# Performance work log

Hardware: AMD Instinct MI355X
Metric: run time of the kernel (lower is better)

## Reference

```python
import jax, jax.numpy as jnp
import numpy as np

D_MODEL = 512
NUM_HEADS = 8
HEAD_DIM = D_MODEL // NUM_HEADS
MAX_REL = 2


def setup_inputs() -> dict:
    key = jax.random.key(0)
    ks = jax.random.split(key, 12)
    B, S = 2, 4096
    std = 1.0 / np.sqrt(D_MODEL)
    inp = {
        'q': jax.random.normal(ks[0], (B, S, D_MODEL), jnp.float32),
        'k': jax.random.normal(ks[1], (B, S, D_MODEL), jnp.float32),
        'v': jax.random.normal(ks[2], (B, S, D_MODEL), jnp.float32),
        'Wq': jax.random.normal(ks[3], (D_MODEL, D_MODEL), jnp.float32) * std,
        'bq': jnp.zeros((D_MODEL,), jnp.float32),
        'Wk': jax.random.normal(ks[4], (D_MODEL, D_MODEL), jnp.float32) * std,
        'bk': jnp.zeros((D_MODEL,), jnp.float32),
        'Wv': jax.random.normal(ks[5], (D_MODEL, D_MODEL), jnp.float32) * std,
        'bv': jnp.zeros((D_MODEL,), jnp.float32),
        'Wo': jax.random.normal(ks[6], (D_MODEL, D_MODEL), jnp.float32) * std,
        'bo': jnp.zeros((D_MODEL,), jnp.float32),
        'rel_pos': jax.random.normal(ks[7], (NUM_HEADS, 2 * MAX_REL + 1), jnp.float32),
    }
    return inp


def _rel_bias(rel_pos, seq_len):
    pos = jnp.arange(seq_len)
    rel = pos[None, :] - pos[:, None]              # [S,S]
    idx = jnp.clip(rel, -MAX_REL, MAX_REL) + MAX_REL
    return rel_pos[:, idx]                         # [H,S,S]


def reference(q, k, v, Wq, bq, Wk, bk, Wv, bv, Wo, bo, rel_pos):
    B, S, D = q.shape
    H, Hd = NUM_HEADS, HEAD_DIM
    # torch Linear: x @ W.T + b
    Q = (q @ Wq.T + bq).reshape(B, S, H, Hd).transpose(0, 2, 1, 3)  # [B,H,S,Hd]
    K = (k @ Wk.T + bk).reshape(B, S, H, Hd).transpose(0, 2, 1, 3)
    V = (v @ Wv.T + bv).reshape(B, S, H, Hd).transpose(0, 2, 1, 3)
    scores = jnp.einsum('bhqd,bhkd->bhqk', Q, K) / jnp.sqrt(jnp.float32(Hd))
    scores = scores + _rel_bias(rel_pos, S)[None]                  # [B,H,S,S]
    probs = jax.nn.softmax(scores, axis=-1)
    attn = jnp.einsum('bhqk,bhkd->bhqd', probs, V)                 # [B,H,S,Hd]
    attn = attn.transpose(0, 2, 1, 3).reshape(B, S, D)
    return attn @ Wo.T + bo
```

## Files before the change

kernel.cpp:

```cpp
#include <hip/hip_runtime.h>

typedef __bf16 bf16_t;
typedef __bf16 bf16x2 __attribute__((ext_vector_type(2)));
typedef __bf16 bf16x4 __attribute__((ext_vector_type(4)));
typedef __bf16 bf16x8 __attribute__((ext_vector_type(8)));
typedef float f32x4 __attribute__((ext_vector_type(4)));
typedef unsigned int u32x4 __attribute__((ext_vector_type(4)));

#define MFMA16(a, b, c) __builtin_amdgcn_mfma_f32_16x16x32_bf16(a, b, c, 0, 0, 0)
#define LOG2E 1.4426950408889634f
#define SHIFT 16.0f

#define GLL(g, l)                                                      \
  __builtin_amdgcn_global_load_lds(                                    \
      (const __attribute__((address_space(1))) void*)(g),              \
      (__attribute__((address_space(3))) void*)(l), 16, 0, 0)

#define WAIT_BARRIER_V4() asm volatile("s_waitcnt vmcnt(4)\n\ts_barrier" ::: "memory")
#define WAIT_BARRIER_V6() asm volatile("s_waitcnt vmcnt(6)\n\ts_barrier" ::: "memory")

static constexpr int NB = 2;
static constexpr int SEQ = 4096;
static constexpr int DM = 512;
static constexpr int NH = 8;
static constexpr int HD = 64;
static constexpr int M_ROWS = NB * SEQ;

__global__ __launch_bounds__(256) void cvt_w_kernel(
    const float* __restrict__ w0, const float* __restrict__ w1,
    const float* __restrict__ w2, const float* __restrict__ w3,
    bf16_t* __restrict__ out) {
  const float* src = (blockIdx.y == 0) ? w0 : (blockIdx.y == 1) ? w1
                   : (blockIdx.y == 2) ? w2 : w3;
  int i = (blockIdx.x * 256 + threadIdx.x) * 4;
  float4 v = *(const float4*)(src + i);
  bf16_t* o = out + blockIdx.y * (DM * DM) + i;
  o[0] = (bf16_t)v.x; o[1] = (bf16_t)v.y; o[2] = (bf16_t)v.z; o[3] = (bf16_t)v.w;
}

__global__ __launch_bounds__(256) void cvt_x_kernel(
    const float* __restrict__ q, const float* __restrict__ k,
    const float* __restrict__ v, bf16_t* __restrict__ out) {
  const float* src = (blockIdx.y == 0) ? q : (blockIdx.y == 1) ? k : v;
  bf16_t* dst = out + (size_t)blockIdx.y * (M_ROWS * DM);
  int i = (blockIdx.x * 256 + threadIdx.x) * 8;
  float4 a = *(const float4*)(src + i);
  float4 b = *(const float4*)(src + i + 4);
  bf16x8 o;
  o[0] = (bf16_t)a.x; o[1] = (bf16_t)a.y; o[2] = (bf16_t)a.z; o[3] = (bf16_t)a.w;
  o[4] = (bf16_t)b.x; o[5] = (bf16_t)b.y; o[6] = (bf16_t)b.z; o[7] = (bf16_t)b.w;
  *(bf16x8*)(dst + i) = o;
}

__device__ __forceinline__ void gemm_body64(
    const bf16_t* __restrict__ X, const bf16_t* __restrict__ Wm,
    const float* __restrict__ bias, void* __restrict__ Out,
    int omode, float scale) {
  __shared__ bf16_t Asm[3][64 * 64];
  __shared__ bf16_t Bsm[3][128 * 64];

  const int tid = threadIdx.x;
  const int w = tid >> 6;
  const int lane = tid & 63;
  const int quad = lane >> 4, l15 = lane & 15;
  const int l8 = lane >> 3;
  const int swcol = ((lane & 7) ^ l8) * 8;
  const int m0 = blockIdx.x * 64;
  const int n0 = blockIdx.y * 128;
  const int moff = (w & 1) * 32;
  const int noff = (w >> 1) * 64;

  f32x4 acc[2][4];
#pragma unroll
  for (int mb = 0; mb < 2; mb++)
#pragma unroll
    for (int nb = 0; nb < 4; nb++) { acc[mb][nb][0] = 0.f; acc[mb][nb][1] = 0.f; acc[mb][nb][2] = 0.f; acc[mb][nb][3] = 0.f; }

  auto stage = [&](int ks, int bufi) {
    const int k0 = ks * 64;
#pragma unroll
    for (int j = 0; j < 4; j++) {
      const int row = j * 32 + w * 8 + l8;
      GLL(Wm + (size_t)(n0 + row) * DM + k0 + swcol, &Bsm[bufi][(j * 256 + w * 64) * 8]);
    }
#pragma unroll
    for (int j = 0; j < 2; j++) {
      const int row = j * 32 + w * 8 + l8;
      GLL(X + (size_t)(m0 + row) * DM + k0 + swcol, &Asm[bufi][(j * 256 + w * 64) * 8]);
    }
  };

  stage(0, 0);
  stage(1, 1);

  for (int ks = 0; ks < 8; ks++) {
    WAIT_BARRIER_V6();
    const int tn = (ks + 2 < 8) ? ks + 2 : 7;
    stage(tn, (ks + 2) % 3);
    const int p = ks % 3;

#pragma unroll
    for (int kd = 0; kd < 2; kd++) {
      const int fch = (((kd << 2) + quad) ^ (l15 & 7)) << 3;
      bf16x8 bfr[4];
#pragma unroll
      for (int nb = 0; nb < 4; nb++)
        bfr[nb] = *(const bf16x8*)&Bsm[p][(noff + nb * 16 + l15) * 64 + fch];
#pragma unroll
      for (int mb = 0; mb < 2; mb++) {
        bf16x8 a = *(const bf16x8*)&Asm[p][(moff + mb * 16 + l15) * 64 + fch];
#pragma unroll
        for (int nb = 0; nb < 4; nb++) acc[mb][nb] = MFMA16(a, bfr[nb], acc[mb][nb]);
      }
    }
  }

#pragma unroll
  for (int nb = 0; nb < 4; nb++) {
    const int n = n0 + noff + nb * 16 + l15;
    const float bn = bias[n];
    const int h = n >> 6, dd = n & 63;
#pragma unroll
    for (int mb = 0; mb < 2; mb++) {
      const int mbase = m0 + moff + mb * 16 + quad * 4;
      const int bb = mbase >> 12, s = mbase & 4095;
      if (omode == 0) {
#pragma unroll
        for (int r = 0; r < 4; r++) {
          const float val = (acc[mb][nb][r] + bn) * scale;
          ((bf16_t*)Out)[(size_t)((bb * NH + h) * SEQ + s + r) * HD + dd] = (bf16_t)val;
        }
      } else if (omode == 1) {
        bf16x4 pk;
#pragma unroll
        for (int r = 0; r < 4; r++) pk[r] = (bf16_t)(acc[mb][nb][r] + bn);
        *(bf16x4*)&((bf16_t*)Out)[(((size_t)(bb * NH + h) * HD + dd) << 12) + s] = pk;
      } else {
#pragma unroll
        for (int r = 0; r < 4; r++)
          ((float*)Out)[(size_t)(mbase + r) * DM + n] = acc[mb][nb][r] + bn;
      }
    }
  }
}

__global__ __launch_bounds__(256, 2) void qkv_kernel(
    const bf16_t* __restrict__ Xall, const bf16_t* __restrict__ Wall,
    const float* __restrict__ bq, const float* __restrict__ bk,
    const float* __restrict__ bv, bf16_t* __restrict__ Qb,
    bf16_t* __restrict__ Kb, bf16_t* __restrict__ Vb, float qscale) {
  const int z = blockIdx.z;
  const bf16_t* X = Xall + (size_t)z * (M_ROWS * DM);
  const float* bias = (z == 0) ? bq : (z == 1) ? bk : bv;
  bf16_t* Out = (z == 0) ? Qb : (z == 1) ? Kb : Vb;
  gemm_body64(X, Wall + (size_t)z * DM * DM, bias, Out,
              (z == 2) ? 1 : 0, (z == 0) ? qscale : 1.0f);
}

__global__ __launch_bounds__(256, 2) void oproj_kernel(
    const bf16_t* __restrict__ X, const bf16_t* __restrict__ Wm,
    const float* __restrict__ bias, float* __restrict__ Out) {
  gemm_body64(X, Wm, bias, Out, 2, 1.0f);
}

__global__ __launch_bounds__(256, 2) void attn_kernel(
    const bf16_t* __restrict__ Qb, const bf16_t* __restrict__ Kb,
    const bf16_t* __restrict__ Vb, const float* __restrict__ rel_pos,
    bf16_t* __restrict__ attn_out) {
  __shared__ bf16_t Kt[3][64 * 64];
  __shared__ bf16_t Vt[3][64 * 64];

  const int tid = threadIdx.x;
  const int w = tid >> 6;
  const int lane = tid & 63;
  const int quad = lane >> 4, l15 = lane & 15;
  const int bh = blockIdx.y;
  const int b = bh >> 3, h = bh & 7;
  const int qlo = blockIdx.x * 128 + w * 32;

  const float rb0 = rel_pos[h * 5 + 0] * LOG2E;
  const float rb1 = rel_pos[h * 5 + 1] * LOG2E;
  const float rb2 = rel_pos[h * 5 + 2] * LOG2E;
  const float rb3 = rel_pos[h * 5 + 3] * LOG2E;
  const float rb4 = rel_pos[h * 5 + 4] * LOG2E;

  bf16x8 qf[2][2];
#pragma unroll
  for (int mb = 0; mb < 2; mb++)
#pragma unroll
    for (int kd = 0; kd < 2; kd++)
      qf[mb][kd] = *(const bf16x8*)(Qb + (size_t)(bh * SEQ + qlo + mb * 16 + l15) * HD + kd * 32 + 8 * quad);

  f32x4 o[2][4];
#pragma unroll
  for (int mb = 0; mb < 2; mb++)
#pragma unroll
    for (int db = 0; db < 4; db++) { o[mb][db][0] = 0.f; o[mb][db][1] = 0.f; o[mb][db][2] = 0.f; o[mb][db][3] = 0.f; }
  f32x4 l4[2];
  l4[0][0] = 0.f; l4[0][1] = 0.f; l4[0][2] = 0.f; l4[0][3] = 0.f;
  l4[1][0] = 0.f; l4[1][1] = 0.f; l4[1][2] = 0.f; l4[1][3] = 0.f;

  bf16x8 ones;
#pragma unroll
  for (int i = 0; i < 8; i++) ones[i] = (bf16_t)1.0f;

  const int srow = (w << 4) + (lane >> 3);
  const int scol = (((lane & 7) ^ (lane >> 3)) << 3);
  const bf16_t* kg0 = Kb + ((size_t)(bh * SEQ + srow) << 6) + scol;
  const bf16_t* vg0 = Vb + (((size_t)(bh * HD + srow)) << 12) + scol;
  const int ldst = (w << 10);

  const int sw = l15 & 7;
  const int kfo0 = (l15 << 6) + ((quad ^ sw) << 3);
  const int kfo1 = (l15 << 6) + (((quad + 4) ^ sw) << 3);

  auto stage = [&](int t, int bufi) {
    GLL(kg0 + ((size_t)t << 12), &Kt[bufi][ldst]);
    GLL(kg0 + ((size_t)t << 12) + (8 << 6), &Kt[bufi][ldst + 512]);
    GLL(vg0 + (t << 6), &Vt[bufi][ldst]);
    GLL(vg0 + (t << 6) + (8 << 12), &Vt[bufi][ldst + 512]);
  };

  stage(0, 0);
  stage(1, 1);

  for (int t = 0; t < 64; t++) {
    WAIT_BARRIER_V4();
    const int tg = (t + 2 < 64) ? t + 2 : 63;
    stage(tg, (t + 2) % 3);
    const int p = t % 3;
    const int kk0 = t * 64;

    float cini;
    bool nearband = false;
    if (kk0 >= qlo + 33) {
      cini = rb4 - SHIFT;
    } else if (kk0 + 63 <= qlo - 2) {
      cini = rb0 - SHIFT;
    } else {
      cini = -SHIFT;
      nearband = true;
    }

    f32x4 s[2][4];
#pragma unroll
    for (int mb = 0; mb < 2; mb++)
#pragma unroll
      for (int kb = 0; kb < 4; kb++) { s[mb][kb][0] = cini; s[mb][kb][1] = cini; s[mb][kb][2] = cini; s[mb][kb][3] = cini; }
    __builtin_amdgcn_s_setprio(1);
#pragma unroll
    for (int kb = 0; kb < 4; kb++) {
      bf16x8 kA0 = *(const bf16x8*)&Kt[p][kfo0 + (kb << 10)];
      bf16x8 kA1 = *(const bf16x8*)&Kt[p][kfo1 + (kb << 10)];
      s[0][kb] = MFMA16(kA0, qf[0][0], s[0][kb]);
      s[0][kb] = MFMA16(kA1, qf[0][1], s[0][kb]);
      s[1][kb] = MFMA16(kA0, qf[1][0], s[1][kb]);
      s[1][kb] = MFMA16(kA1, qf[1][1], s[1][kb]);
    }
    __builtin_amdgcn_s_setprio(0);

    if (nearband) {
#pragma unroll
      for (int mb = 0; mb < 2; mb++) {
        const int qg = qlo + mb * 16 + l15;
#pragma unroll
        for (int kb = 0; kb < 4; kb++)
#pragma unroll
          for (int r = 0; r < 4; r++) {
            int dl = kk0 + kb * 16 + quad * 4 + r - qg;
            float bias = dl <= -2 ? rb0
                       : (dl >= 2 ? rb4
                       : (dl == -1 ? rb1 : (dl == 0 ? rb2 : rb3)));
            s[mb][kb][r] += bias;
          }
      }
    }

    bf16x8 pf[2][2];
#pragma unroll
    for (int mb = 0; mb < 2; mb++) {
      unsigned int u[4][2];
#pragma unroll
      for (int kb = 0; kb < 4; kb++) {
        bf16x2 p0, p1;
        p0[0] = (bf16_t)__builtin_amdgcn_exp2f(s[mb][kb][0]);
        p0[1] = (bf16_t)__builtin_amdgcn_exp2f(s[mb][kb][1]);
        p1[0] = (bf16_t)__builtin_amdgcn_exp2f(s[mb][kb][2]);
        p1[1] = (bf16_t)__builtin_amdgcn_exp2f(s[mb][kb][3]);
        u[kb][0] = __builtin_bit_cast(unsigned int, p0);
        u[kb][1] = __builtin_bit_cast(unsigned int, p1);
      }
#pragma unroll
      for (int kc = 0; kc < 2; kc++) {
        unsigned int a0 = u[2 * kc][0], b0 = u[2 * kc + 1][0];
        unsigned int a1 = u[2 * kc][1], b1 = u[2 * kc + 1][1];
        asm("v_permlane32_swap_b32 %0, %1" : "+v"(a0), "+v"(b0));
        asm("v_permlane32_swap_b32 %0, %1" : "+v"(a1), "+v"(b1));
        asm("v_permlane16_swap_b32 %0, %1" : "+v"(a0), "+v"(b0));
        asm("v_permlane16_swap_b32 %0, %1" : "+v"(a1), "+v"(b1));
        u32x4 pk; pk[0] = a0; pk[1] = a1; pk[2] = b0; pk[3] = b1;
        pf[mb][kc] = __builtin_bit_cast(bf16x8, pk);
      }
    }

    __builtin_amdgcn_s_setprio(1);
    l4[0] = MFMA16(ones, pf[0][0], l4[0]);
    l4[0] = MFMA16(ones, pf[0][1], l4[0]);
    l4[1] = MFMA16(ones, pf[1][0], l4[1]);
    l4[1] = MFMA16(ones, pf[1][1], l4[1]);

#pragma unroll
    for (int db = 0; db < 4; db++) {
      bf16x8 vA0 = *(const bf16x8*)&Vt[p][kfo0 + (db << 10)];
      bf16x8 vA1 = *(const bf16x8*)&Vt[p][kfo1 + (db << 10)];
      o[0][db] = MFMA16(vA0, pf[0][0], o[0][db]);
      o[0][db] = MFMA16(vA1, pf[0][1], o[0][db]);
      o[1][db] = MFMA16(vA0, pf[1][0], o[1][db]);
      o[1][db] = MFMA16(vA1, pf[1][1], o[1][db]);
    }
    __builtin_amdgcn_s_setprio(0);
  }

#pragma unroll
  for (int mb = 0; mb < 2; mb++) {
    const float inv = 1.0f / l4[mb][0];
    const int qg = qlo + mb * 16 + l15;
#pragma unroll
    for (int db = 0; db < 4; db++) {
      bf16x4 pk;
#pragma unroll
      for (int r = 0; r < 4; r++) pk[r] = (bf16_t)(o[mb][db][r] * inv);
      *(bf16x4*)(attn_out + (size_t)(b * SEQ + qg) * DM + h * HD + db * 16 + quad * 4) = pk;
    }
  }
}

extern "C" void kernel_launch(void* const* d_in, const int* in_sizes, int n_in,
                              void* d_out, int out_size, void* d_ws, size_t ws_size,
                              hipStream_t stream) {
  const float* q   = (const float*)d_in[0];
  const float* k   = (const float*)d_in[1];
  const float* v   = (const float*)d_in[2];
  const float* Wq  = (const float*)d_in[3];
  const float* bq  = (const float*)d_in[4];
  const float* Wk  = (const float*)d_in[5];
  const float* bk  = (const float*)d_in[6];
  const float* Wv  = (const float*)d_in[7];
  const float* bv  = (const float*)d_in[8];
  const float* Wo  = (const float*)d_in[9];
  const float* bo  = (const float*)d_in[10];
  const float* rel = (const float*)d_in[11];

  char* ws = (char*)d_ws;
  bf16_t* Wbf  = (bf16_t*)ws;
  bf16_t* Xb   = (bf16_t*)(ws + (size_t)(2  << 20));
  bf16_t* Qbuf = (bf16_t*)(ws + (size_t)(26 << 20));
  bf16_t* Kbuf = (bf16_t*)(ws + (size_t)(34 << 20));
  bf16_t* Vbuf = (bf16_t*)(ws + (size_t)(42 << 20));
  bf16_t* Abuf = (bf16_t*)(ws + (size_t)(2  << 20));

  cvt_w_kernel<<<dim3(256, 4), 256, 0, stream>>>(Wq, Wk, Wv, Wo, Wbf);
  cvt_x_kernel<<<dim3(2048, 3), 256, 0, stream>>>(q, k, v, Xb);

  const float qscale = LOG2E / 8.0f;
  qkv_kernel<<<dim3(128, 4, 3), 256, 0, stream>>>(
      Xb, Wbf, bq, bk, bv, Qbuf, Kbuf, Vbuf, qscale);

  attn_kernel<<<dim3(32, 16), 256, 0, stream>>>(Qbuf, Kbuf, Vbuf, rel, Abuf);

  oproj_kernel<<<dim3(128, 4), 256, 0, stream>>>(Abuf, Wbf + 3 * DM * DM, bo, (float*)d_out);
}
```

Measured before the change: 235.9 us.

## Software-pipeline QK^T one tile ahead of softmax/PV with 4-deep LDS ring

Restructures the attention main loop so the QK^T MFMAs for tile t+1 are issued before the softmax and PV work of tile t, using two ping-ponged score register sets. The LDS K/V ring grows from 3 to 4 buffers and prefetch distance from 2 to 3 tiles. The grid is flattened to 1D with a remap that interleaves (batch, head, q-block) assignment across XCDs for L2 locality. The aim is to overlap exp/VALU work with matrix-core work and hide load latency, at the cost of more registers and LDS, which may reduce occupancy.

```diff
diff --git a/kernel.cpp b/kernel.cpp
--- a/kernel.cpp
+++ b/kernel.cpp
@@ -18,6 +18,7 @@
 
 #define WAIT_BARRIER_V4() asm volatile("s_waitcnt vmcnt(4)\n\ts_barrier" ::: "memory")
 #define WAIT_BARRIER_V6() asm volatile("s_waitcnt vmcnt(6)\n\ts_barrier" ::: "memory")
+#define WAIT_BARRIER_V8() asm volatile("s_waitcnt vmcnt(8)\n\ts_barrier" ::: "memory")
 
 static constexpr int NB = 2;
 static constexpr int SEQ = 4096;
@@ -167,16 +168,20 @@
     const bf16_t* __restrict__ Qb, const bf16_t* __restrict__ Kb,
     const bf16_t* __restrict__ Vb, const float* __restrict__ rel_pos,
     bf16_t* __restrict__ attn_out) {
-  __shared__ bf16_t Kt[3][64 * 64];
-  __shared__ bf16_t Vt[3][64 * 64];
+  __shared__ bf16_t Kt[4][64 * 64];
+  __shared__ bf16_t Vt[4][64 * 64];
 
   const int tid = threadIdx.x;
   const int w = tid >> 6;
   const int lane = tid & 63;
   const int quad = lane >> 4, l15 = lane & 15;
-  const int bh = blockIdx.y;
+
+  const int lin = blockIdx.x;
+  const int glob = (lin & 7) * 64 + (lin >> 3);
+  const int bh = glob >> 5;
+  const int qb = glob & 31;
   const int b = bh >> 3, h = bh & 7;
-  const int qlo = blockIdx.x * 128 + w * 32;
+  const int qlo = qb * 128 + w * 32;
 
   const float rb0 = rel_pos[h * 5 + 0] * LOG2E;
   const float rb1 = rel_pos[h * 5 + 1] * LOG2E;
@@ -221,44 +226,33 @@
     GLL(vg0 + (t << 6) + (8 << 12), &Vt[bufi][ldst + 512]);
   };
 
-  stage(0, 0);
-  stage(1, 1);
-
-  for (int t = 0; t < 64; t++) {
-    WAIT_BARRIER_V4();
-    const int tg = (t + 2 < 64) ? t + 2 : 63;
-    stage(tg, (t + 2) % 3);
-    const int p = t % 3;
-    const int kk0 = t * 64;
-
+  auto qk_tile = [&](int tq, f32x4 (&s)[2][4]) {
+    const int kk0 = tq * 64;
     float cini;
-    bool nearband = false;
-    if (kk0 >= qlo + 33) {
-      cini = rb4 - SHIFT;
-    } else if (kk0 + 63 <= qlo - 2) {
-      cini = rb0 - SHIFT;
-    } else {
-      cini = -SHIFT;
-      nearband = true;
-    }
-
-    f32x4 s[2][4];
+    if (kk0 >= qlo + 33)            cini = rb4 - SHIFT;
+    else if (kk0 + 63 <= qlo - 2)   cini = rb0 - SHIFT;
+    else                            cini = -SHIFT;
 #pragma unroll
     for (int mb = 0; mb < 2; mb++)
 #pragma unroll
       for (int kb = 0; kb < 4; kb++) { s[mb][kb][0] = cini; s[mb][kb][1] = cini; s[mb][kb][2] = cini; s[mb][kb][3] = cini; }
+    const int pq = tq & 3;
     __builtin_amdgcn_s_setprio(1);
 #pragma unroll
     for (int kb = 0; kb < 4; kb++) {
-      bf16x8 kA0 = *(const bf16x8*)&Kt[p][kfo0 + (kb << 10)];
-      bf16x8 kA1 = *(const bf16x8*)&Kt[p][kfo1 + (kb << 10)];
+      bf16x8 kA0 = *(const bf16x8*)&Kt[pq][kfo0 + (kb << 10)];
+      bf16x8 kA1 = *(const bf16x8*)&Kt[pq][kfo1 + (kb << 10)];
       s[0][kb] = MFMA16(kA0, qf[0][0], s[0][kb]);
       s[0][kb] = MFMA16(kA1, qf[0][1], s[0][kb]);
       s[1][kb] = MFMA16(kA0, qf[1][0], s[1][kb]);
       s[1][kb] = MFMA16(kA1, qf[1][1], s[1][kb]);
     }
     __builtin_amdgcn_s_setprio(0);
-
+  };
+
+  auto sm_pv = [&](int t, f32x4 (&s)[2][4]) {
+    const int kk0 = t * 64;
+    const bool nearband = !(kk0 >= qlo + 33) && !(kk0 + 63 <= qlo - 2);
     if (nearband) {
 #pragma unroll
       for (int mb = 0; mb < 2; mb++) {
@@ -303,12 +297,12 @@
       }
     }
 
+    const int p = t & 3;
     __builtin_amdgcn_s_setprio(1);
     l4[0] = MFMA16(ones, pf[0][0], l4[0]);
     l4[0] = MFMA16(ones, pf[0][1], l4[0]);
     l4[1] = MFMA16(ones, pf[1][0], l4[1]);
     l4[1] = MFMA16(ones, pf[1][1], l4[1]);
-
 #pragma unroll
     for (int db = 0; db < 4; db++) {
       bf16x8 vA0 = *(const bf16x8*)&Vt[p][kfo0 + (db << 10)];
@@ -319,6 +313,33 @@
       o[1][db] = MFMA16(vA1, pf[1][1], o[1][db]);
     }
     __builtin_amdgcn_s_setprio(0);
+  };
+
+  stage(0, 0);
+  stage(1, 1);
+  stage(2, 2);
+  WAIT_BARRIER_V8();
+
+  f32x4 sA[2][4], sB[2][4];
+  qk_tile(0, sA);
+
+  for (int t2 = 0; t2 < 32; t2++) {
+    {
+      const int t = 2 * t2;
+      WAIT_BARRIER_V4();
+      const int tg = (t + 3 < 64) ? t + 3 : 63;
+      stage(tg, (t + 3) & 3);
+      qk_tile(t + 1, sB);
+      sm_pv(t, sA);
+    }
+    {
+      const int t = 2 * t2 + 1;
+      WAIT_BARRIER_V4();
+      const int tg = (t + 3 < 64) ? t + 3 : 63;
+      stage(tg, (t + 3) & 3);
+      if (t < 63) qk_tile(t + 1, sA);
+      sm_pv(t, sB);
+    }
   }
 
 #pragma unroll
@@ -366,7 +387,7 @@
   qkv_kernel<<<dim3(128, 4, 3), 256, 0, stream>>>(
       Xb, Wbf, bq, bk, bv, Qbuf, Kbuf, Vbuf, qscale);
 
-  attn_kernel<<<dim3(32, 16), 256, 0, stream>>>(Qbuf, Kbuf, Vbuf, rel, Abuf);
+  attn_kernel<<<512, 256, 0, stream>>>(Qbuf, Kbuf, Vbuf, rel, Abuf);
 
   oproj_kernel<<<dim3(128, 4), 256, 0, stream>>>(Abuf, Wbf + 3 * DM * DM, bo, (float*)d_out);
 }
```

Result: no change. 232.7 us (-1.3%).
